# Optimization experiments

Hardware: AMD Instinct MI355X
Metric: run time of the kernel (lower is better)

## Reference

```python
import jax, jax.numpy as jnp
import numpy as np

K = 7  # SMorph filter size


def _smorph(x, w, alpha):
    # x: [B,1,H,W]; w: [K,K]; alpha: scalar
    # SMorph(x)(p) = sum_s (x(p+s)+w(s)) * exp(alpha*(x(p+s)+w(s))) / sum_s exp(...)
    patches = jax.lax.conv_general_dilated_patches(
        x, filter_shape=(K, K), window_strides=(1, 1), padding='SAME')  # [B,K*K,H,W]
    z = patches + w.reshape(1, K * K, 1, 1)
    wts = jax.nn.softmax(alpha * z, axis=1)
    out = jnp.sum(z * wts, axis=1, keepdims=True)  # [B,1,H,W]
    return out


def _pool2(x):
    # 2x2 average pool, stride 2; x: [...,H,W]
    B, C, H, W = x.shape
    return x.reshape(B, C, H // 2, 2, W // 2, 2).mean(axis=(3, 5))


def setup_inputs() -> dict:
    key = jax.random.key(0)
    ks = jax.random.split(key, 9)
    B = 512
    return {
        'x': jax.random.normal(ks[0], (B, 1, 28, 28), dtype=jnp.float32),
        'sm_w': 0.5 * jax.random.normal(ks[1], (8, 2, K, K), dtype=jnp.float32),
        'sm_alpha': jax.random.uniform(ks[2], (8, 2), dtype=jnp.float32),
        'W1': jax.random.normal(ks[3], (120, 392), dtype=jnp.float32) / np.sqrt(392),
        'b1': jax.random.normal(ks[4], (120,), dtype=jnp.float32) * 0.01,
        'W2': jax.random.normal(ks[5], (84, 120), dtype=jnp.float32) / np.sqrt(120),
        'b2': jax.random.normal(ks[6], (84,), dtype=jnp.float32) * 0.01,
        'W3': jax.random.normal(ks[7], (10, 84), dtype=jnp.float32) / np.sqrt(84),
        'b3': jax.random.normal(ks[8], (10,), dtype=jnp.float32) * 0.01,
    }


def reference(x, sm_w, sm_alpha, W1, b1, W2, b2, W3, b3):
    B = x.shape[0]

    def branch(w2, a2):
        y = _smorph(x, w2[0], a2[0])
        y = _smorph(y, w2[1], a2[1])
        y = _pool2(_pool2(y))  # [B,1,7,7]
        return y

    ys = jax.vmap(branch)(sm_w, sm_alpha)  # [8,B,1,7,7]
    feat = jnp.transpose(ys, (1, 0, 2, 3, 4)).reshape(B, -1)  # [B,392] = concat(x1..x8)
    h = jax.nn.sigmoid(feat @ W1.T + b1)
    h = jax.nn.sigmoid(h @ W2.T + b2)
    out = jax.nn.sigmoid(h @ W3.T + b3)
    return out
```

## Files before the change

### kernel.cpp

```cpp
#include <hip/hip_runtime.h>

#define HW 28
#define NPIX 784
#define NB 512
#define PADW2 34
#define PADH 34
#define IMG_F2 (PADH * PADW2)

__device__ __forceinline__ void conv2col(const float2* sbuf,
                                         const unsigned* wlds,
                                         int R0, int c, float o0[7], float o1[7])
{
    unsigned Wh[49];
    {
        const uint4* wp = (const uint4*)wlds;
#pragma unroll
        for (int k = 0; k < 12; ++k) {
            uint4 q = wp[k];
            Wh[4 * k + 0] = q.x; Wh[4 * k + 1] = q.y;
            Wh[4 * k + 2] = q.z; Wh[4 * k + 3] = q.w;
        }
        Wh[48] = wlds[48];
    }

    float num0[7], num1[7], den0[7], den1[7];
#pragma unroll
    for (int r = 0; r < 7; ++r) {
        num0[r] = 0.f; num1[r] = 0.f; den0[r] = 0.f; den1[r] = 0.f;
    }

#pragma unroll
    for (int rr = 0; rr < 13; ++rr) {
        const float4* rq = (const float4*)(sbuf + (R0 + rr) * PADW2 + 2 * c);
        float4 q0 = rq[0], q1 = rq[1], q2 = rq[2], q3 = rq[3];
        float ev[8] = {q0.x, q0.z, q1.x, q1.z, q2.x, q2.z, q3.x, q3.z};
        float pv[8] = {q0.y, q0.w, q1.y, q1.w, q2.y, q2.w, q3.y, q3.w};
#pragma unroll
        for (int r = 0; r < 7; ++r) {
            if (r > rr || rr - r > 6) continue;
            const int di = rr - r;
#pragma unroll
            for (int t = 0; t < 7; ++t) {
                unsigned w = Wh[di * 7 + t];
                float t1a, t1b;
                asm("v_fma_mix_f32 %0, %1, %2, %3 op_sel_hi:[1,0,0]"
                    : "=v"(t1a) : "v"(w), "v"(ev[t]),     "v"(pv[t]));
                asm("v_fma_mix_f32 %0, %1, %2, %3 op_sel_hi:[1,0,0]"
                    : "=v"(t1b) : "v"(w), "v"(ev[t + 1]), "v"(pv[t + 1]));
                asm("v_fma_mix_f32 %0, %1, %2, %0 op_sel:[1,0,0] op_sel_hi:[1,0,0]"
                    : "+v"(num0[r]) : "v"(w), "v"(t1a));
                asm("v_fma_mix_f32 %0, %1, %2, %0 op_sel:[1,0,0] op_sel_hi:[1,0,0]"
                    : "+v"(num1[r]) : "v"(w), "v"(t1b));
                asm("v_fma_mix_f32 %0, %1, %2, %0 op_sel:[1,0,0] op_sel_hi:[1,0,0]"
                    : "+v"(den0[r]) : "v"(w), "v"(ev[t]));
                asm("v_fma_mix_f32 %0, %1, %2, %0 op_sel:[1,0,0] op_sel_hi:[1,0,0]"
                    : "+v"(den1[r]) : "v"(w), "v"(ev[t + 1]));
            }
        }
    }
#pragma unroll
    for (int r = 0; r < 7; ++r) {
        o0[r] = num0[r] * __builtin_amdgcn_rcpf(den0[r]);
        o1[r] = num1[r] * __builtin_amdgcn_rcpf(den1[r]);
    }
}

__device__ __forceinline__ float sigmoidf_(float s) {
    return __builtin_amdgcn_rcpf(1.f + __expf(-s));
}

__global__ __launch_bounds__(512, 2) void smorph_net_kernel(
    const float* __restrict__ x,
    const float* __restrict__ sw,
    const float* __restrict__ sa,
    const float* __restrict__ W1, const float* __restrict__ b1,
    const float* __restrict__ W2, const float* __restrict__ b2,
    const float* __restrict__ W3, const float* __restrict__ b3,
    float* __restrict__ out)
{
    __shared__ __align__(16) float2   bufs[8][IMG_F2];
    __shared__ __align__(16) unsigned wtab[8][2][52];

    const int b    = blockIdx.x;
    const int tid  = threadIdx.x;
    const int f    = tid >> 6;
    const int lane = tid & 63;

    float2* buf = bufs[f];
    const float* src = x + (size_t)b * NPIX;

    const float a1 = sa[f * 2 + 0];
    const float a2 = sa[f * 2 + 1];

    if (lane < 49) {
        union { _Float16 h[2]; unsigned u; } p;
        float w1v = sw[(f * 2 + 0) * 49 + lane];
        p.h[0] = (_Float16)w1v;
        p.h[1] = (_Float16)__expf(a1 * w1v);
        wtab[f][0][lane] = p.u;
        float w2v = sw[(f * 2 + 1) * 49 + lane];
        p.h[0] = (_Float16)w2v;
        p.h[1] = (_Float16)__expf(a2 * w2v);
        wtab[f][1][lane] = p.u;
    }

    for (int idx = lane; idx < IMG_F2; idx += 64) {
        int pi = idx / PADW2;
        int pj = idx - pi * PADW2;
        float2 val = make_float2(1.f, 0.f);
        if (pi >= 3 && pi < 31 && pj >= 3 && pj < 31) {
            float v = src[(pi - 3) * HW + (pj - 3)];
            float e = __expf(a1 * v);
            val = make_float2(e, v * e);
        }
        buf[idx] = val;
    }

    const bool act = (lane < 56);
    const int s  = lane / 14;
    const int c  = lane - s * 14;
    const int R0 = 7 * s;
    const int j2 = 2 * c;

    float o0[7], o1[7];
    if (act) conv2col(buf, wtab[f][0], R0, c, o0, o1);

    if (act) {
#pragma unroll
        for (int r = 0; r < 7; ++r) {
            float e0 = __expf(a2 * o0[r]);
            float e1 = __expf(a2 * o1[r]);
            buf[(R0 + r + 3) * PADW2 + (j2 + 3)] = make_float2(e0, o0[r] * e0);
            buf[(R0 + r + 3) * PADW2 + (j2 + 4)] = make_float2(e1, o1[r] * e1);
        }
    }

    if (act) conv2col(buf, wtab[f][1], R0, c, o0, o1);

    float* outp = (float*)buf;
    if (act) {
#pragma unroll
        for (int r = 0; r < 7; ++r) {
            outp[(R0 + r) * HW + j2]     = o0[r];
            outp[(R0 + r) * HW + j2 + 1] = o1[r];
        }
    }

    float poolsum = 0.f;
    if (lane < 49) {
        int pi = lane / 7;
        int pj = lane - pi * 7;
#pragma unroll
        for (int di = 0; di < 4; ++di)
#pragma unroll
            for (int dj = 0; dj < 4; ++dj)
                poolsum += outp[(pi * 4 + di) * HW + (pj * 4 + dj)];
        poolsum *= 0.0625f;
    }
    __syncthreads();

    float* feat = (float*)&wtab[0][0][0];
    float* h1   = feat + 392;
    float* h2   = h1 + 120;

    if (lane < 49) feat[f * 49 + lane] = poolsum;
    __syncthreads();

    if (tid < 480) {
        int n = tid >> 2, h = tid & 3;
        const float4* wr = (const float4*)(W1 + n * 392);
        const float4* fv = (const float4*)feat;
        float c0 = 0.f, c1 = 0.f, c2 = 0.f, c3 = 0.f;
        for (int k = h; k < 98; k += 4) {
            float4 w = wr[k];
            float4 v = fv[k];
            c0 = fmaf(w.x, v.x, c0);
            c1 = fmaf(w.y, v.y, c1);
            c2 = fmaf(w.z, v.z, c2);
            c3 = fmaf(w.w, v.w, c3);
        }
        float acc = (c0 + c1) + (c2 + c3);
        acc += __shfl_xor(acc, 1);
        acc += __shfl_xor(acc, 2);
        if (h == 0) h1[n] = sigmoidf_(acc + b1[n]);
    }
    __syncthreads();

    if (tid < 336) {
        int n = tid >> 2, h = tid & 3;
        const float4* wr = (const float4*)(W2 + n * 120);
        const float4* hv = (const float4*)h1;
        float c0 = 0.f, c1 = 0.f, c2 = 0.f, c3 = 0.f;
        for (int k = h; k < 30; k += 4) {
            float4 w = wr[k];
            float4 v = hv[k];
            c0 = fmaf(w.x, v.x, c0);
            c1 = fmaf(w.y, v.y, c1);
            c2 = fmaf(w.z, v.z, c2);
            c3 = fmaf(w.w, v.w, c3);
        }
        float acc = (c0 + c1) + (c2 + c3);
        acc += __shfl_xor(acc, 1);
        acc += __shfl_xor(acc, 2);
        if (h == 0) h2[n] = sigmoidf_(acc + b2[n]);
    }
    __syncthreads();

    if (tid < 40) {
        int n = tid >> 2, q = tid & 3;
        const float4* wr = (const float4*)(W3 + n * 84);
        const float4* hv = (const float4*)h2;
        float c0 = 0.f, c1 = 0.f, c2 = 0.f, c3 = 0.f;
        for (int k = q; k < 21; k += 4) {
            float4 w = wr[k];
            float4 v = hv[k];
            c0 = fmaf(w.x, v.x, c0);
            c1 = fmaf(w.y, v.y, c1);
            c2 = fmaf(w.z, v.z, c2);
            c3 = fmaf(w.w, v.w, c3);
        }
        float acc = (c0 + c1) + (c2 + c3);
        acc += __shfl_xor(acc, 1);
        acc += __shfl_xor(acc, 2);
        if (q == 0) out[(size_t)b * 10 + n] = sigmoidf_(acc + b3[n]);
    }
}

extern "C" void kernel_launch(void* const* d_in, const int* in_sizes, int n_in,
                              void* d_out, int out_size, void* d_ws, size_t ws_size,
                              hipStream_t stream) {
    const float* x  = (const float*)d_in[0];
    const float* sw = (const float*)d_in[1];
    const float* sa = (const float*)d_in[2];
    const float* W1 = (const float*)d_in[3];
    const float* b1 = (const float*)d_in[4];
    const float* W2 = (const float*)d_in[5];
    const float* b2 = (const float*)d_in[6];
    const float* W3 = (const float*)d_in[7];
    const float* b3 = (const float*)d_in[8];
    float* out = (float*)d_out;

    smorph_net_kernel<<<NB, 512, 0, stream>>>(x, sw, sa, W1, b1, W2, b2, W3, b3, out);
}
```

Baseline: 113.9 us.

## Pack image planes as fp16 pairs and use dot2 for numerator accumulation

The padded image buffer now stores exp(a*x) and x*exp(a*x) as packed fp16 pairs in one 32-bit word instead of a float2. The weight table is reordered so each numerator term becomes one v_dot2_f32_f16, replacing two fma_mix instructions. This halves LDS footprint and read traffic and cuts the inner-loop instruction count from six to four per tap pair. The cost is fp16 rounding of image values and products, which risks overflow for large exponents and lower accuracy.

After: 102.8 us. 9.7% less time.

```diff
diff --git a/kernel.cpp b/kernel.cpp
--- a/kernel.cpp
+++ b/kernel.cpp
@@ -5,9 +5,9 @@
 #define NB 512
 #define PADW2 34
 #define PADH 34
-#define IMG_F2 (PADH * PADW2)
-
-__device__ __forceinline__ void conv2col(const float2* sbuf,
+#define IMG_U (PADH * PADW2)
+
+__device__ __forceinline__ void conv2col(const unsigned* sbuf,
                                          const unsigned* wlds,
                                          int R0, int c, float o0[7], float o1[7])
 {
@@ -31,30 +31,24 @@
 
 #pragma unroll
     for (int rr = 0; rr < 13; ++rr) {
-        const float4* rq = (const float4*)(sbuf + (R0 + rr) * PADW2 + 2 * c);
-        float4 q0 = rq[0], q1 = rq[1], q2 = rq[2], q3 = rq[3];
-        float ev[8] = {q0.x, q0.z, q1.x, q1.z, q2.x, q2.z, q3.x, q3.z};
-        float pv[8] = {q0.y, q0.w, q1.y, q1.w, q2.y, q2.w, q3.y, q3.w};
+        const uint2* rq = (const uint2*)(sbuf + (R0 + rr) * PADW2 + 2 * c);
+        uint2 a0 = rq[0], a1 = rq[1], a2 = rq[2], a3 = rq[3];
+        unsigned tp[8] = {a0.x, a0.y, a1.x, a1.y, a2.x, a2.y, a3.x, a3.y};
 #pragma unroll
         for (int r = 0; r < 7; ++r) {
             if (r > rr || rr - r > 6) continue;
             const int di = rr - r;
 #pragma unroll
             for (int t = 0; t < 7; ++t) {
-                unsigned w = Wh[di * 7 + t];
-                float t1a, t1b;
-                asm("v_fma_mix_f32 %0, %1, %2, %3 op_sel_hi:[1,0,0]"
-                    : "=v"(t1a) : "v"(w), "v"(ev[t]),     "v"(pv[t]));
-                asm("v_fma_mix_f32 %0, %1, %2, %3 op_sel_hi:[1,0,0]"
-                    : "=v"(t1b) : "v"(w), "v"(ev[t + 1]), "v"(pv[t + 1]));
-                asm("v_fma_mix_f32 %0, %1, %2, %0 op_sel:[1,0,0] op_sel_hi:[1,0,0]"
-                    : "+v"(num0[r]) : "v"(w), "v"(t1a));
-                asm("v_fma_mix_f32 %0, %1, %2, %0 op_sel:[1,0,0] op_sel_hi:[1,0,0]"
-                    : "+v"(num1[r]) : "v"(w), "v"(t1b));
-                asm("v_fma_mix_f32 %0, %1, %2, %0 op_sel:[1,0,0] op_sel_hi:[1,0,0]"
-                    : "+v"(den0[r]) : "v"(w), "v"(ev[t]));
-                asm("v_fma_mix_f32 %0, %1, %2, %0 op_sel:[1,0,0] op_sel_hi:[1,0,0]"
-                    : "+v"(den1[r]) : "v"(w), "v"(ev[t + 1]));
+                unsigned wq = Wh[di * 7 + t];
+                asm("v_dot2_f32_f16 %0, %1, %2, %0"
+                    : "+v"(num0[r]) : "v"(tp[t]),     "v"(wq));
+                asm("v_dot2_f32_f16 %0, %1, %2, %0"
+                    : "+v"(num1[r]) : "v"(tp[t + 1]), "v"(wq));
+                asm("v_fma_mix_f32 %0, %1, %2, %0 op_sel:[1,0,0] op_sel_hi:[1,1,0]"
+                    : "+v"(den0[r]) : "v"(wq), "v"(tp[t]));
+                asm("v_fma_mix_f32 %0, %1, %2, %0 op_sel:[1,0,0] op_sel_hi:[1,1,0]"
+                    : "+v"(den1[r]) : "v"(wq), "v"(tp[t + 1]));
             }
         }
     }
@@ -78,7 +72,7 @@
     const float* __restrict__ W3, const float* __restrict__ b3,
     float* __restrict__ out)
 {
-    __shared__ __align__(16) float2   bufs[8][IMG_F2];
+    __shared__ __align__(16) unsigned bufs[8][IMG_U];
     __shared__ __align__(16) unsigned wtab[8][2][52];
 
     const int b    = blockIdx.x;
@@ -86,7 +80,7 @@
     const int f    = tid >> 6;
     const int lane = tid & 63;
 
-    float2* buf = bufs[f];
+    unsigned* buf = bufs[f];
     const float* src = x + (size_t)b * NPIX;
 
     const float a1 = sa[f * 2 + 0];
@@ -95,23 +89,28 @@
     if (lane < 49) {
         union { _Float16 h[2]; unsigned u; } p;
         float w1v = sw[(f * 2 + 0) * 49 + lane];
-        p.h[0] = (_Float16)w1v;
-        p.h[1] = (_Float16)__expf(a1 * w1v);
+        float e1  = __expf(a1 * w1v);
+        p.h[0] = (_Float16)(w1v * e1);
+        p.h[1] = (_Float16)e1;
         wtab[f][0][lane] = p.u;
         float w2v = sw[(f * 2 + 1) * 49 + lane];
-        p.h[0] = (_Float16)w2v;
-        p.h[1] = (_Float16)__expf(a2 * w2v);
+        float e2  = __expf(a2 * w2v);
+        p.h[0] = (_Float16)(w2v * e2);
+        p.h[1] = (_Float16)e2;
         wtab[f][1][lane] = p.u;
     }
 
-    for (int idx = lane; idx < IMG_F2; idx += 64) {
+    for (int idx = lane; idx < IMG_U; idx += 64) {
         int pi = idx / PADW2;
         int pj = idx - pi * PADW2;
-        float2 val = make_float2(1.f, 0.f);
+        unsigned val = 0x00003C00u;
         if (pi >= 3 && pi < 31 && pj >= 3 && pj < 31) {
             float v = src[(pi - 3) * HW + (pj - 3)];
             float e = __expf(a1 * v);
-            val = make_float2(e, v * e);
+            union { _Float16 h[2]; unsigned u; } pk;
+            pk.h[0] = (_Float16)e;
+            pk.h[1] = (_Float16)(v * e);
+            val = pk.u;
         }
         buf[idx] = val;
     }
@@ -128,10 +127,13 @@
     if (act) {
 #pragma unroll
         for (int r = 0; r < 7; ++r) {
+            union { _Float16 h[2]; unsigned u; } pk;
             float e0 = __expf(a2 * o0[r]);
+            pk.h[0] = (_Float16)e0; pk.h[1] = (_Float16)(o0[r] * e0);
+            buf[(R0 + r + 3) * PADW2 + (j2 + 3)] = pk.u;
             float e1 = __expf(a2 * o1[r]);
-            buf[(R0 + r + 3) * PADW2 + (j2 + 3)] = make_float2(e0, o0[r] * e0);
-            buf[(R0 + r + 3) * PADW2 + (j2 + 4)] = make_float2(e1, o1[r] * e1);
+            pk.h[0] = (_Float16)e1; pk.h[1] = (_Float16)(o1[r] * e1);
+            buf[(R0 + r + 3) * PADW2 + (j2 + 4)] = pk.u;
         }
     }
 
```
